# Optimization experiments

Hardware: AMD Instinct MI355X
Metric: run time of the kernel (lower is better)

Reference implementation:

```python
import jax, jax.numpy as jnp
import numpy as np

GAMMA = 1.0
LAMBDA = 0.5
CLAMP = (-10.0, 10.0)


def setup_inputs() -> dict:
    key = jax.random.key(0)
    k1, k2, k3 = jax.random.split(key, 3)
    m, S, D = 64, 4096, 128
    generated_samples = jax.random.normal(k1, (m, S, D), dtype=jnp.float32)
    target_sample = jax.random.normal(k2, (S, D), dtype=jnp.float32)
    time_points = jax.random.uniform(k3, (S,), dtype=jnp.float32)
    return {
        "generated_samples": generated_samples,
        "target_sample": target_sample,
        "time_points": time_points,
    }


def reference(generated_samples, target_sample, time_points):
    # paths = concat([time, values], -1); since time_points is shared across all
    # paths, the time column cancels in path_i - path_j, so the RBF kernel
    # k(x,y)=exp(-gamma*||x-y||^2) depends only on the value tensors.
    m = generated_samples.shape[0]
    X = generated_samples.reshape(m, -1)          # [m, S*D]
    t = target_sample.reshape(-1)                 # [S*D]

    # Pairwise squared distances via gram trick (one pass over X, tiny GEMM).
    sq = jnp.sum(X * X, axis=1)                   # [m]
    gram = X @ X.T                                # [m, m]
    d2 = jnp.maximum(sq[:, None] + sq[None, :] - 2.0 * gram, 0.0)
    K = jnp.exp(-GAMMA * d2)                      # [m, m]
    # off-diagonal sum (diag of K is exp(0)=1 -> subtract m)
    cross_sum = jnp.sum(K) - jnp.trace(K)
    cross_term = (LAMBDA / 2.0) * cross_sum / (m * (m - 1))

    # E[k(X, Y)] against target
    dt2 = jnp.sum((X - t[None, :]) ** 2, axis=1)  # [m]
    target_term = jnp.mean(jnp.exp(-GAMMA * dt2))

    score = cross_term - target_term
    return jnp.clip(score, CLAMP[0], CLAMP[1])
```

## Files before the change

kernel.cpp:

```cpp
#include <hip/hip_runtime.h>
#include <hip/hip_bf16.h>

#define NROW 65
#define GP   80
#define GE   (GP * GP)
#define BK   128
#define ROWB (BK * 4)
#define RPAD 80
#define BUFB (RPAD * ROWB)
#define TPB  256
#define GRID_MAX 512

typedef float  f32x4  __attribute__((ext_vector_type(4)));
typedef __bf16 bf16x8 __attribute__((ext_vector_type(8)));

__device__ __forceinline__ void gl_lds16(const void* g, void* l) {
  __builtin_amdgcn_global_load_lds(
      (const __attribute__((address_space(1))) void*)g,
      (__attribute__((address_space(3))) void*)l, 16, 0, 0);
}

__global__ __launch_bounds__(TPB) void gram_k(
    const float* __restrict__ X,
    const float* __restrict__ T,
    float* __restrict__ S,
    int Nk, int nch)
{
  __shared__ __align__(16) char smem[2 * BUFB];
  const int tid  = threadIdx.x;
  const int wv   = tid >> 6;
  const int lane = tid & 63;
  const int l32  = lane & 31, half = lane >> 5;
  const int lr   = lane & 15, kg = lane >> 4;

  f32x4 acc[15];
#pragma unroll
  for (int i = 0; i < 15; ++i) acc[i] = (f32x4){0.f, 0.f, 0.f, 0.f};

  auto stage = [&](char* buf, int c) {
#pragma unroll
    for (int i = 0; i < 8; ++i) {
      const int p   = wv + 4 * i;
      const int r0  = 2 * p;
      const int row = r0 + half;
      const char* src = (const char*)(X + (size_t)row * Nk + (size_t)c * BK)
                        + (((l32 * 16) ^ ((row & 7) << 4)));
      gl_lds16(src, buf + r0 * ROWB);
    }
    if (wv == 0 && lane < 32) {
      const char* src = (const char*)(T + (size_t)c * BK) + l32 * 16;
      gl_lds16(src, buf + 64 * ROWB);
    }
  };

  int c = blockIdx.x;
  stage(smem, c);
  int it = 0;
  while (true) {
    char* cur = smem + (it & 1) * BUFB;
    char* nxt = smem + ((it & 1) ^ 1) * BUFB;
    const int cn = c + gridDim.x;
    const bool has_next = cn < nch;
    if (has_next) stage(nxt, cn);

    if (has_next) {
      if (wv == 0) asm volatile("s_waitcnt vmcnt(9)" ::: "memory");
      else         asm volatile("s_waitcnt vmcnt(8)" ::: "memory");
    } else {
      asm volatile("s_waitcnt vmcnt(0)" ::: "memory");
    }
    __builtin_amdgcn_sched_barrier(0);
    __builtin_amdgcn_s_barrier();
    __builtin_amdgcn_sched_barrier(0);

    {
      const int inner = wv * 128 + kg * 32;
      bf16x8 f[5];
#pragma unroll
      for (int t = 0; t < 5; ++t) {
        const int row = t * 16 + lr;
        const char* base = cur + row * ROWB;
        const int swz = (row & 7) << 4;
        f32x4 a = *(const f32x4*)(base + (inner ^ swz));
        f32x4 b = *(const f32x4*)(base + ((inner + 16) ^ swz));
        f[t] = (bf16x8){(__bf16)a.x, (__bf16)a.y, (__bf16)a.z, (__bf16)a.w,
                        (__bf16)b.x, (__bf16)b.y, (__bf16)b.z, (__bf16)b.w};
      }
#pragma unroll
      for (int I = 0; I < 5; ++I)
#pragma unroll
        for (int J = I; J < 5; ++J) {
          const int idx = I * 5 + J - (I * (I + 1)) / 2;
          acc[idx] = __builtin_amdgcn_mfma_f32_16x16x32_bf16(f[I], f[J], acc[idx], 0, 0, 0);
        }
    }
    __builtin_amdgcn_s_barrier();
    if (!has_next) break;
    c = cn; ++it;
  }

  float* gl = (float*)smem;
  __syncthreads();
  for (int e = tid; e < GE; e += TPB) gl[e] = 0.f;
  __syncthreads();
  for (int w = 0; w < 4; ++w) {
    if (wv == w) {
#pragma unroll
      for (int I = 0; I < 5; ++I)
#pragma unroll
        for (int J = I; J < 5; ++J) {
          const int idx = I * 5 + J - (I * (I + 1)) / 2;
#pragma unroll
          for (int r = 0; r < 4; ++r) {
            const int grow = I * 16 + kg * 4 + r;
            const int gcol = J * 16 + lr;
            gl[grow * GP + gcol] += acc[idx][r];
          }
        }
    }
    __syncthreads();
  }
  float* dst = S + (size_t)blockIdx.x * GE;
  for (int e = tid; e < GE; e += TPB) dst[e] = gl[e];
}

#define RBLK 64
__global__ __launch_bounds__(256) void reduce_k(
    const float* __restrict__ S, float* __restrict__ G, int nsl)
{
  __shared__ float ps[4][RBLK];
  const int tid = threadIdx.x;
  const int e0  = blockIdx.x * RBLK;
  const int el  = tid & (RBLK - 1);
  const int p   = tid >> 6;
  const float* base = S + (size_t)p * GE + (e0 + el);
  float s = 0.f;
  int i = p;
#pragma unroll 8
  for (; i + 32 <= nsl; i += 32) {
    s += base[0];
    s += base[(size_t)4  * GE];
    s += base[(size_t)8  * GE];
    s += base[(size_t)12 * GE];
    s += base[(size_t)16 * GE];
    s += base[(size_t)20 * GE];
    s += base[(size_t)24 * GE];
    s += base[(size_t)28 * GE];
    base += (size_t)32 * GE;
  }
  for (; i < nsl; i += 4) { s += base[0]; base += (size_t)4 * GE; }
  ps[p][el] = s;
  __syncthreads();
  if (tid < RBLK)
    G[e0 + tid] = ps[0][tid] + ps[1][tid] + ps[2][tid] + ps[3][tid];
}

__global__ __launch_bounds__(256) void epilogue_k(
    const float* __restrict__ G, float* __restrict__ out)
{
  __shared__ float gl[GE];
  __shared__ float rx[4], rt[4];
  const int tid = threadIdx.x;
  for (int e = tid; e < GE; e += 256) gl[e] = G[e];
  __syncthreads();

  float accX = 0.f, accT = 0.f;
  for (int e = tid; e < GE; e += 256) {
    int i = e / GP, j = e % GP;
    if (j >= NROW || i >= j) continue;
    float g  = gl[e];
    float d2 = gl[i * GP + i] + gl[j * GP + j] - 2.f * g;
    if (j < 64) accX += expf(-fmaxf(d2, 0.f));
    else        accT += expf(-d2);
  }
#pragma unroll
  for (int off = 32; off > 0; off >>= 1) {
    accX += __shfl_down(accX, off);
    accT += __shfl_down(accT, off);
  }
  const int wv = tid >> 6, lane = tid & 63;
  if (lane == 0) { rx[wv] = accX; rt[wv] = accT; }
  __syncthreads();
  if (tid == 0) {
    float sx = rx[0] + rx[1] + rx[2] + rx[3];
    float st = rt[0] + rt[1] + rt[2] + rt[3];
    float score = sx / 8064.f - st / 64.f;
    score = fminf(fmaxf(score, -10.f), 10.f);
    out[0] = score;
  }
}

extern "C" void kernel_launch(void* const* d_in, const int* in_sizes, int n_in,
                              void* d_out, int out_size, void* d_ws, size_t ws_size,
                              hipStream_t stream) {
  const float* X = (const float*)d_in[0];
  const float* T = (const float*)d_in[1];
  float* out = (float*)d_out;

  const int Nk  = in_sizes[1];
  const int nch = Nk / BK;

  int nsl = (int)(ws_size / (GE * sizeof(float))) - 1;
  if (nsl > GRID_MAX) nsl = GRID_MAX;
  if (nsl < 1) nsl = 1;
  float* S = (float*)d_ws;
  float* G = S + (size_t)nsl * GE;

  gram_k<<<nsl, TPB, 0, stream>>>(X, T, S, Nk, nch);
  reduce_k<<<(GE / RBLK), 256, 0, stream>>>(S, G, nsl);
  epilogue_k<<<1, 256, 0, stream>>>(G, out);
}
```

Before: 211.1 us.

## Give each wave private double-buffered chunks to remove block barriers

Each wave now streams its own 32-column chunk of X and the target row into a private double buffer in LDS, replacing the block-wide 128-column chunk shared by four waves. This drops the two workgroup barriers per iteration, so waves no longer stall on each other while loads land. In exchange each global load covers a narrower 128-byte row segment, the chunk count grows fourfold, and each wave runs more loop iterations with more waitcnt overhead per MFMA.

Measured after the change: 210.0 us. About the same (-0.5%).

```diff
diff --git a/kernel.cpp b/kernel.cpp
--- a/kernel.cpp
+++ b/kernel.cpp
@@ -4,10 +4,11 @@
 #define NROW 65
 #define GP   80
 #define GE   (GP * GP)
-#define BK   128
-#define ROWB (BK * 4)
-#define RPAD 80
-#define BUFB (RPAD * ROWB)
+#define CHF  32
+#define ROWB 128
+#define NRB  66
+#define BUFB (NRB * ROWB)
+#define WBUF (2 * BUFB)
 #define TPB  256
 #define GRID_MAX 512
 
@@ -26,76 +27,69 @@
     float* __restrict__ S,
     int Nk, int nch)
 {
-  __shared__ __align__(16) char smem[2 * BUFB];
+  __shared__ __align__(16) char smem[4 * WBUF];
   const int tid  = threadIdx.x;
   const int wv   = tid >> 6;
   const int lane = tid & 63;
-  const int l32  = lane & 31, half = lane >> 5;
   const int lr   = lane & 15, kg = lane >> 4;
+  const size_t Nkb = (size_t)Nk * 4;
+
+  char* myb = smem + wv * WBUF;
 
   f32x4 acc[15];
 #pragma unroll
   for (int i = 0; i < 15; ++i) acc[i] = (f32x4){0.f, 0.f, 0.f, 0.f};
 
   auto stage = [&](char* buf, int c) {
+    const size_t colb = (size_t)c * ROWB;
 #pragma unroll
     for (int i = 0; i < 8; ++i) {
-      const int p   = wv + 4 * i;
-      const int r0  = 2 * p;
-      const int row = r0 + half;
-      const char* src = (const char*)(X + (size_t)row * Nk + (size_t)c * BK)
-                        + (((l32 * 16) ^ ((row & 7) << 4)));
-      gl_lds16(src, buf + r0 * ROWB);
-    }
-    if (wv == 0 && lane < 32) {
-      const char* src = (const char*)(T + (size_t)c * BK) + l32 * 16;
+      const int r  = 8 * i + (lane >> 3);
+      const int ss = (lane & 7) ^ ((lane >> 3) & 7);
+      const char* src = (const char*)X + (size_t)r * Nkb + colb + ss * 16;
+      gl_lds16(src, buf + i * 1024);
+    }
+    if (lane < 8) {
+      const char* src = (const char*)T + colb + lane * 16;
       gl_lds16(src, buf + 64 * ROWB);
     }
   };
 
-  int c = blockIdx.x;
-  stage(smem, c);
+  const int nwaves = gridDim.x * (TPB / 64);
+  int c = blockIdx.x * (TPB / 64) + wv;
+  stage(myb, c);
   int it = 0;
   while (true) {
-    char* cur = smem + (it & 1) * BUFB;
-    char* nxt = smem + ((it & 1) ^ 1) * BUFB;
-    const int cn = c + gridDim.x;
-    const bool has_next = cn < nch;
-    if (has_next) stage(nxt, cn);
-
-    if (has_next) {
-      if (wv == 0) asm volatile("s_waitcnt vmcnt(9)" ::: "memory");
-      else         asm volatile("s_waitcnt vmcnt(8)" ::: "memory");
-    } else {
-      asm volatile("s_waitcnt vmcnt(0)" ::: "memory");
-    }
+    char* cur = myb + (it & 1) * BUFB;
+    char* nxt = myb + ((it & 1) ^ 1) * BUFB;
+    const int cn = c + nwaves;
+    const bool hn = cn < nch;
+    asm volatile("s_waitcnt lgkmcnt(0)" ::: "memory");
     __builtin_amdgcn_sched_barrier(0);
-    __builtin_amdgcn_s_barrier();
+    if (hn) stage(nxt, cn);
+    if (hn) asm volatile("s_waitcnt vmcnt(9)" ::: "memory");
+    else    asm volatile("s_waitcnt vmcnt(0)" ::: "memory");
     __builtin_amdgcn_sched_barrier(0);
 
-    {
-      const int inner = wv * 128 + kg * 32;
-      bf16x8 f[5];
-#pragma unroll
-      for (int t = 0; t < 5; ++t) {
-        const int row = t * 16 + lr;
-        const char* base = cur + row * ROWB;
-        const int swz = (row & 7) << 4;
-        f32x4 a = *(const f32x4*)(base + (inner ^ swz));
-        f32x4 b = *(const f32x4*)(base + ((inner + 16) ^ swz));
-        f[t] = (bf16x8){(__bf16)a.x, (__bf16)a.y, (__bf16)a.z, (__bf16)a.w,
-                        (__bf16)b.x, (__bf16)b.y, (__bf16)b.z, (__bf16)b.w};
+    bf16x8 f[5];
+#pragma unroll
+    for (int t = 0; t < 5; ++t) {
+      int r = t * 16 + lr; if (r > 65) r = 65;
+      const char* rb = cur + r * ROWB;
+      const int sw = (r & 7) << 4;
+      f32x4 a = *(const f32x4*)(rb + ((kg * 32) ^ sw));
+      f32x4 b = *(const f32x4*)(rb + ((kg * 32 + 16) ^ sw));
+      f[t] = (bf16x8){(__bf16)a.x, (__bf16)a.y, (__bf16)a.z, (__bf16)a.w,
+                      (__bf16)b.x, (__bf16)b.y, (__bf16)b.z, (__bf16)b.w};
+    }
+#pragma unroll
+    for (int I = 0; I < 5; ++I)
+#pragma unroll
+      for (int J = I; J < 5; ++J) {
+        const int idx = I * 5 + J - (I * (I + 1)) / 2;
+        acc[idx] = __builtin_amdgcn_mfma_f32_16x16x32_bf16(f[I], f[J], acc[idx], 0, 0, 0);
       }
-#pragma unroll
-      for (int I = 0; I < 5; ++I)
-#pragma unroll
-        for (int J = I; J < 5; ++J) {
-          const int idx = I * 5 + J - (I * (I + 1)) / 2;
-          acc[idx] = __builtin_amdgcn_mfma_f32_16x16x32_bf16(f[I], f[J], acc[idx], 0, 0, 0);
-        }
-    }
-    __builtin_amdgcn_s_barrier();
-    if (!has_next) break;
+    if (!hn) break;
     c = cn; ++it;
   }
 
@@ -198,7 +192,7 @@
   float* out = (float*)d_out;
 
   const int Nk  = in_sizes[1];
-  const int nch = Nk / BK;
+  const int nch = Nk / CHF;
 
   int nsl = (int)(ws_size / (GE * sizeof(float))) - 1;
   if (nsl > GRID_MAX) nsl = GRID_MAX;
```
